# Optimization experiments

Measured on AMD Instinct MI355X. Metric: run time of the kernel, lower is better.

## Reference

```python
import jax, jax.numpy as jnp
import numpy as np

NEG_INF = -1e30
EPS = 1e-7  # keras.backend.epsilon()


def _ctc_loss(y_true, y_pred):
    """Faithful CTC loss matching keras ctc_batch_cost + tf v1 ctc_loss.

    y_true: [B, L] int labels (no blanks), all rows full length L.
    y_pred: [B, T, C] probabilities; tf ctc_loss re-softmaxes log(p+eps).
    Blank index = C - 1. Returns loss [B, 1].
    """
    B, T, C = y_pred.shape
    L = y_true.shape[1]
    S = 2 * L + 1
    blank = C - 1

    # keras passes log(y_pred+eps) as logits; tf ctc_loss applies softmax
    lp = jax.nn.log_softmax(jnp.log(y_pred + EPS), axis=-1)  # [B,T,C]

    # extended label sequence: blank, l0, blank, l1, ..., blank  [B,S]
    ext = jnp.full((B, S), blank, dtype=y_true.dtype)
    ext = ext.at[:, 1::2].set(y_true)

    # skip transition (s-2 -> s) allowed iff ext[s] != blank and ext[s] != ext[s-2]
    same_as_2back = jnp.concatenate(
        [jnp.ones((B, 2), bool), ext[:, 2:] == ext[:, :-2]], axis=1)
    can_skip = (ext != blank) & (~same_as_2back)  # [B,S]

    # emission log-prob of each lattice state at each time: [B,T,S]
    lp_ext = jnp.take_along_axis(lp, ext[:, None, :], axis=2)

    # alpha init at t=0: only states 0 (blank) and 1 (first label) reachable
    alpha0 = jnp.full((B, S), NEG_INF, dtype=lp.dtype)
    alpha0 = alpha0.at[:, 0].set(lp_ext[:, 0, 0])
    alpha0 = alpha0.at[:, 1].set(lp_ext[:, 0, 1])

    pad1 = jnp.full((B, 1), NEG_INF, dtype=lp.dtype)
    pad2 = jnp.full((B, 2), NEG_INF, dtype=lp.dtype)

    def step(alpha, lp_t):
        a_stay = alpha
        a_prev = jnp.concatenate([pad1, alpha[:, :-1]], axis=1)
        a_skip = jnp.where(can_skip,
                           jnp.concatenate([pad2, alpha[:, :-2]], axis=1),
                           NEG_INF)
        m = jnp.maximum(a_stay, jnp.maximum(a_prev, a_skip))
        lse = m + jnp.log(jnp.exp(a_stay - m) + jnp.exp(a_prev - m)
                          + jnp.exp(a_skip - m))
        return lse + lp_t, None

    # scan over remaining T-1 time steps
    alphaT, _ = jax.lax.scan(step, alpha0, jnp.swapaxes(lp_ext, 0, 1)[1:])

    # total log-likelihood: end at last blank or last label
    loglik = jnp.logaddexp(alphaT[:, S - 1], alphaT[:, S - 2])
    return -loglik[:, None]  # [B,1], matches expand_dims(..., 1)


def setup_inputs() -> dict:
    key = jax.random.key(0)
    k1, k2 = jax.random.split(key)
    B, T, C, L = 128, 1024, 128, 128
    y_true = jax.random.randint(k1, (B, L), 0, C - 1, dtype=jnp.int32)
    y_pred = jax.random.uniform(k2, (B, T, C), dtype=jnp.float32)
    return {"y_true": y_true, "y_pred": y_pred}


def reference(y_true, y_pred):
    return _ctc_loss(y_true, y_pred)
```

## Files before the change

kernel.cpp:

```cpp
#include <hip/hip_runtime.h>

#define TT 1024
#define CC 128
#define LL 128
#define EPSF 1e-7f
#define LN2F 0.69314718055994531f

#define LOG2F(x) __builtin_amdgcn_logf(x)

typedef unsigned int uint;

template <int CTRL>
__device__ __forceinline__ int dpp_i(int old_, int x) {
  return __builtin_amdgcn_update_dpp(old_, x, CTRL, 0xf, 0xf, false);
}
__device__ __forceinline__ float dpp_shr1_f32(float x) {
  return __uint_as_float((uint)__builtin_amdgcn_update_dpp(
      0, (int)__float_as_uint(x), 0x138, 0xf, 0xf, true));
}

__device__ __forceinline__ uint bf16bits(float x) {
  uint u = __float_as_uint(x);
  return (u + 0x7fffu + ((u >> 16) & 1u)) >> 16;
}

__device__ __forceinline__ float bperm(int byteaddr, float v) {
  return __uint_as_float(
      (uint)__builtin_amdgcn_ds_bpermute(byteaddr, (int)__float_as_uint(v)));
}


#define CTC_STEP(wv, pbf)                                   \
  do {                                                      \
    const float p1 = __uint_as_float((wv) << 16);           \
    const float p2 = __uint_as_float((wv) & 0xffff0000u);   \
    const float pb = (pbf);                                 \
    const float p3 = dpp_shr1_f32(a3);                      \
    const float n0 = (a0 + p3) * pb;                        \
    const float n1 = __builtin_fmaf(s1f, p3, a0 + a1) * p1; \
    const float n2 = (a2 + a1) * pb;                        \
    const float n3 = __builtin_fmaf(s3f, a1, a3 + a2) * p2; \
    const float n4 = (a4 + a3) * pb;                        \
    a0 = n0; a1 = n1; a2 = n2; a3 = n3; a4 = n4;            \
  } while (0)

#define CTC_QUAD(et, eb)      \
  do {                        \
    CTC_STEP((et).x, (eb).x); \
    CTC_STEP((et).y, (eb).y); \
    CTC_STEP((et).z, (eb).z); \
    CTC_STEP((et).w, (eb).w); \
  } while (0)

#define CTC_RESCALE()                                                \
  do {                                                               \
    const float m = fmaxf(fmaxf(fmaxf(a0, a1), fmaxf(a2, a3)), a4);  \
    int ke = (int)(__float_as_uint(m) >> 23);                        \
    ke = max(ke, dpp_i<0x111>(ke, ke));                              \
    ke = max(ke, dpp_i<0x112>(ke, ke));                              \
    ke = max(ke, dpp_i<0x114>(ke, ke));                              \
    ke = max(ke, dpp_i<0x118>(ke, ke));                              \
    ke = max(ke, dpp_i<0x142>(ke, ke));                              \
    ke = max(ke, dpp_i<0x143>(ke, ke));                              \
    ke = __builtin_amdgcn_readlane(ke, 63);                          \
    int e = ke - 227;             \
    e = e < -127 ? -127 : e;                                         \
    const float sc = __uint_as_float((uint)(127 - e) << 23);         \
    a0 *= sc; a1 *= sc; a2 *= sc; a3 *= sc; a4 *= sc;                \
    ell += e;                                                        \
  } while (0)

#define STAGE8(t0)                                                          \
  do {                                                                      \
    float2 vv[8];                                                           \
    _Pragma("unroll") for (int j = 0; j < 8; ++j)                           \
        vv[j] = *(const float2*)(Pb + (size_t)((t0) + j) * CC);             \
    _Pragma("unroll") for (int q = 0; q < 2; ++q) {                         \
      uint wds[4];                                                          \
      float nys[4];                                                         \
      _Pragma("unroll") for (int c = 0; c < 4; ++c) {                       \
        const int j = q * 4 + c;                                            \
        float x = (vv[j].x + EPSF) + (vv[j].y + EPSF);                      \
        _Pragma("unroll") for (int off = 32; off > 0; off >>= 1)            \
            x += __shfl_xor(x, off);                                        \
        const float r = 1.0f / x;                                           \
        const float er = EPSF * r;                                          \
        const float nx = __builtin_fmaf(vv[j].x, r, er);                    \
        const float ny = __builtin_fmaf(vv[j].y, r, er);                    \
        const float c1a = bperm(gxb, nx), c1b = bperm(gxb, ny);             \
        const float c2a = bperm(gyb, nx), c2b = bperm(gyb, ny);             \
        const float g1 = sx ? c1b : c1a;                                    \
        const float g2 = sy ? c2b : c2a;                                    \
        wds[c] = (bf16bits(g2) << 16) | bf16bits(g1);                       \
        nys[c] = ny;                                                        \
      }                                                                     \
      const int tq = (t0) + q * 4;                                          \
      uint4 val;                                                            \
      val.x = wds[0]; val.y = wds[1]; val.z = wds[2]; val.w = wds[3];       \
      *(uint4*)((char*)ETl + ((tq >> 5) & 3) * 8192 +                       \
                ((tq >> 2) & 7) * 1024 + L * 16) = val;                     \
      if (L == 63) {                                                        \
        float4 e4;                                                          \
        e4.x = nys[0]; e4.y = nys[1]; e4.z = nys[2]; e4.w = nys[3];         \
        *(float4*)&EBl[tq] = e4;                                            \
      }                                                                     \
    }                                                                       \
  } while (0)

__global__ __launch_bounds__(320) void ctc_fused(const int* __restrict__ yt,
                                                 const float* __restrict__ yp,
                                                 float* __restrict__ out) {
  const int b = blockIdx.x;
  const int tid = threadIdx.x;
  const int L = tid & 63;
  const int w = tid >> 6;

  __shared__ uint4 ETl[4][8][64];
  __shared__ __align__(16) float EBl[TT];

  const int2 lab = *(const int2*)(yt + b * LL + 2 * L);

  const int labm1 = __shfl_up(lab.y, 1);
  const float s1f = ((L > 0) && (lab.x != labm1)) ? 1.0f : 0.0f;
  const float s3f = (lab.y != lab.x) ? 1.0f : 0.0f;

  const float* Pb = yp + (size_t)b * TT * CC + 2 * L;
  const int gxb = (lab.x >> 1) << 2, gyb = (lab.y >> 1) << 2;
  const int sx = lab.x & 1, sy = lab.y & 1;

  if (w != 0) {
    STAGE8((w - 1) * 8);
    STAGE8(32 + (w - 1) * 8);
  }
  __syncthreads();

  uint4 etA = {0, 0, 0, 0}, etB = {0, 0, 0, 0};
  float4 ebA = {0, 0, 0, 0}, ebB = {0, 0, 0, 0};
  if (w == 0) {
    etA = ((const uint4*)ETl)[L];
    ebA = *(const float4*)&EBl[0];
  }

  float a0 = (w == 0 && L == 0) ? 0x1.0p100f : 0.0f;
  float a1 = 0.0f, a2 = 0.0f, a3 = 0.0f, a4 = 0.0f;
  int ell = -100;

#pragma unroll 1
  for (int kk = 0; kk < 32; ++kk) {
    if (w == 0) {
      const uint4* cur = (const uint4*)ETl + (size_t)(kk & 3) * 512;
      const float4* ebp = (const float4*)&EBl[kk * 32];
      etB = cur[1 * 64 + L]; ebB = ebp[1];
      CTC_QUAD(etA, ebA);
      etA = cur[2 * 64 + L]; ebA = ebp[2];
      CTC_QUAD(etB, ebB);
      etB = cur[3 * 64 + L]; ebB = ebp[3];
      CTC_QUAD(etA, ebA);
      etA = cur[4 * 64 + L]; ebA = ebp[4];
      CTC_QUAD(etB, ebB);
      CTC_RESCALE();
      etB = cur[5 * 64 + L]; ebB = ebp[5];
      CTC_QUAD(etA, ebA);
      etA = cur[6 * 64 + L]; ebA = ebp[6];
      CTC_QUAD(etB, ebB);
      etB = cur[7 * 64 + L]; ebB = ebp[7];
      CTC_QUAD(etA, ebA);
      etA = ((const uint4*)ETl)[(size_t)((kk + 1) & 3) * 512 + L];
      ebA = *(const float4*)&EBl[(kk < 31) ? (kk + 1) * 32 : 1020];
      CTC_QUAD(etB, ebB);
      CTC_RESCALE();
    } else if (kk < 30) {
      STAGE8((kk + 2) * 32 + (w - 1) * 8);
    }
    __syncthreads();
  }

  if (tid == 63) {
    float s = a3 + a4;
    if (s < 1e-37f) s = 1e-37f;
    out[b] = -LN2F * ((float)ell + LOG2F(s));
  }
}

extern "C" void kernel_launch(void* const* d_in, const int* in_sizes, int n_in,
                              void* d_out, int out_size, void* d_ws,
                              size_t ws_size, hipStream_t stream) {
  (void)d_ws; (void)ws_size; (void)n_in; (void)out_size;
  const int* yt = (const int*)d_in[0];
  const float* yp = (const float*)d_in[1];
  float* out = (float*)d_out;
  const int B = in_sizes[0] / LL;
  hipLaunchKernelGGL(ctc_fused, dim3(B), dim3(320), 0, stream, yt, yp, out);
}
```

Before: 155.6 us.

## Use direct label gathers and DPP row-sum, cut producer waves to three

The staging path stops permuting normalized probabilities across lanes with ds_bpermute. Each lane now loads its two label columns straight from global memory. The row sum over 128 classes uses a DPP reduction plus readlane instead of xor shuffles, with four rows batched for more instruction parallelism. The block shrinks from five waves to four (one recurrence wave, three producers), and work is redistributed in 4-row groups. The aim is lower per-row staging latency, so fewer producer waves can keep up with the alpha recurrence, at the cost of extra scattered global loads and less producer parallelism.

New measurement: 149.7 us. 1.04x faster.

```diff
diff --git a/kernel.cpp b/kernel.cpp
--- a/kernel.cpp
+++ b/kernel.cpp
@@ -14,19 +14,23 @@
 __device__ __forceinline__ int dpp_i(int old_, int x) {
   return __builtin_amdgcn_update_dpp(old_, x, CTRL, 0xf, 0xf, false);
 }
+template <int CTRL>
+__device__ __forceinline__ float dpp0f(float x) {
+  return __uint_as_float((uint)__builtin_amdgcn_update_dpp(
+      0, (int)__float_as_uint(x), CTRL, 0xf, 0xf, true));
+}
 __device__ __forceinline__ float dpp_shr1_f32(float x) {
   return __uint_as_float((uint)__builtin_amdgcn_update_dpp(
       0, (int)__float_as_uint(x), 0x138, 0xf, 0xf, true));
 }
+__device__ __forceinline__ float readlane63_f(float v) {
+  return __uint_as_float(
+      (uint)__builtin_amdgcn_readlane((int)__float_as_uint(v), 63));
+}
 
 __device__ __forceinline__ uint bf16bits(float x) {
   uint u = __float_as_uint(x);
   return (u + 0x7fffu + ((u >> 16) & 1u)) >> 16;
-}
-
-__device__ __forceinline__ float bperm(int byteaddr, float v) {
-  return __uint_as_float(
-      (uint)__builtin_amdgcn_ds_bpermute(byteaddr, (int)__float_as_uint(v)));
 }
 
 
@@ -70,44 +74,55 @@
     ell += e;                                                        \
   } while (0)
 
-#define STAGE8(t0)                                                          \
-  do {                                                                      \
-    float2 vv[8];                                                           \
-    _Pragma("unroll") for (int j = 0; j < 8; ++j)                           \
-        vv[j] = *(const float2*)(Pb + (size_t)((t0) + j) * CC);             \
-    _Pragma("unroll") for (int q = 0; q < 2; ++q) {                         \
-      uint wds[4];                                                          \
-      float nys[4];                                                         \
-      _Pragma("unroll") for (int c = 0; c < 4; ++c) {                       \
-        const int j = q * 4 + c;                                            \
-        float x = (vv[j].x + EPSF) + (vv[j].y + EPSF);                      \
-        _Pragma("unroll") for (int off = 32; off > 0; off >>= 1)            \
-            x += __shfl_xor(x, off);                                        \
-        const float r = 1.0f / x;                                           \
-        const float er = EPSF * r;                                          \
-        const float nx = __builtin_fmaf(vv[j].x, r, er);                    \
-        const float ny = __builtin_fmaf(vv[j].y, r, er);                    \
-        const float c1a = bperm(gxb, nx), c1b = bperm(gxb, ny);             \
-        const float c2a = bperm(gyb, nx), c2b = bperm(gyb, ny);             \
-        const float g1 = sx ? c1b : c1a;                                    \
-        const float g2 = sy ? c2b : c2a;                                    \
-        wds[c] = (bf16bits(g2) << 16) | bf16bits(g1);                       \
-        nys[c] = ny;                                                        \
-      }                                                                     \
-      const int tq = (t0) + q * 4;                                          \
-      uint4 val;                                                            \
-      val.x = wds[0]; val.y = wds[1]; val.z = wds[2]; val.w = wds[3];       \
-      *(uint4*)((char*)ETl + ((tq >> 5) & 3) * 8192 +                       \
-                ((tq >> 2) & 7) * 1024 + L * 16) = val;                     \
-      if (L == 63) {                                                        \
-        float4 e4;                                                          \
-        e4.x = nys[0]; e4.y = nys[1]; e4.z = nys[2]; e4.w = nys[3];         \
-        *(float4*)&EBl[tq] = e4;                                            \
-      }                                                                     \
-    }                                                                       \
-  } while (0)
-
-__global__ __launch_bounds__(320) void ctc_fused(const int* __restrict__ yt,
+#define STAGE4(qg)                                                        \
+  do {                                                                    \
+    const int t0 = (qg) * 4;                                              \
+    float2 vv[4];                                                         \
+    float gx[4], gy[4];                                                   \
+    _Pragma("unroll") for (int j = 0; j < 4; ++j) {                       \
+      const float* Pr = Pb + (size_t)(t0 + j) * CC;                       \
+      vv[j] = *(const float2*)(Pr + 2 * L);                               \
+      gx[j] = Pr[labx];                                                   \
+      gy[j] = Pr[laby];                                                   \
+    }                                                                     \
+    float ss[4];                                                          \
+    _Pragma("unroll") for (int j = 0; j < 4; ++j)                         \
+        ss[j] = (vv[j].x + vv[j].y) + (2.0f * EPSF);                      \
+    _Pragma("unroll") for (int j = 0; j < 4; ++j)                         \
+        ss[j] += dpp0f<0x111>(ss[j]);                      \
+    _Pragma("unroll") for (int j = 0; j < 4; ++j)                         \
+        ss[j] += dpp0f<0x112>(ss[j]);                      \
+    _Pragma("unroll") for (int j = 0; j < 4; ++j)                         \
+        ss[j] += dpp0f<0x114>(ss[j]);                      \
+    _Pragma("unroll") for (int j = 0; j < 4; ++j)                         \
+        ss[j] += dpp0f<0x118>(ss[j]);                      \
+    _Pragma("unroll") for (int j = 0; j < 4; ++j)                         \
+        ss[j] += dpp0f<0x142>(ss[j]);                    \
+    _Pragma("unroll") for (int j = 0; j < 4; ++j)                         \
+        ss[j] += dpp0f<0x143>(ss[j]);  \
+    uint wds[4];                                                          \
+    float nys[4];                                                         \
+    _Pragma("unroll") for (int j = 0; j < 4; ++j) {                       \
+      const float x = readlane63_f(ss[j]);                                \
+      const float r = 1.0f / x;                                           \
+      const float er = EPSF * r;                                          \
+      const float g1 = __builtin_fmaf(gx[j], r, er);                      \
+      const float g2 = __builtin_fmaf(gy[j], r, er);                      \
+      wds[j] = (bf16bits(g2) << 16) | bf16bits(g1);                       \
+      nys[j] = __builtin_fmaf(vv[j].y, r, er);                            \
+    }                                                                     \
+    uint4 val;                                                            \
+    val.x = wds[0]; val.y = wds[1]; val.z = wds[2]; val.w = wds[3];       \
+    *(uint4*)((char*)ETl + (((qg) >> 3) & 3) * 8192 +                     \
+              ((qg) & 7) * 1024 + L * 16) = val;                          \
+    if (L == 63) {                                                        \
+      float4 e4;                                                          \
+      e4.x = nys[0]; e4.y = nys[1]; e4.z = nys[2]; e4.w = nys[3];         \
+      *(float4*)&EBl[t0] = e4;                                            \
+    }                                                                     \
+  } while (0)
+
+__global__ __launch_bounds__(256) void ctc_fused(const int* __restrict__ yt,
                                                  const float* __restrict__ yp,
                                                  float* __restrict__ out) {
   const int b = blockIdx.x;
@@ -124,13 +139,11 @@
   const float s1f = ((L > 0) && (lab.x != labm1)) ? 1.0f : 0.0f;
   const float s3f = (lab.y != lab.x) ? 1.0f : 0.0f;
 
-  const float* Pb = yp + (size_t)b * TT * CC + 2 * L;
-  const int gxb = (lab.x >> 1) << 2, gyb = (lab.y >> 1) << 2;
-  const int sx = lab.x & 1, sy = lab.y & 1;
+  const float* Pb = yp + (size_t)b * TT * CC;
+  const int labx = lab.x, laby = lab.y;
 
   if (w != 0) {
-    STAGE8((w - 1) * 8);
-    STAGE8(32 + (w - 1) * 8);
+    for (int q = w - 1; q < 16; q += 3) STAGE4(q);
   }
   __syncthreads();
 
@@ -170,7 +183,7 @@
       CTC_QUAD(etB, ebB);
       CTC_RESCALE();
     } else if (kk < 30) {
-      STAGE8((kk + 2) * 32 + (w - 1) * 8);
+      for (int q = w - 1; q < 8; q += 3) STAGE4((kk + 2) * 8 + q);
     }
     __syncthreads();
   }
@@ -190,5 +203,5 @@
   const float* yp = (const float*)d_in[1];
   float* out = (float*)d_out;
   const int B = in_sizes[0] / LL;
-  hipLaunchKernelGGL(ctc_fused, dim3(B), dim3(320), 0, stream, yt, yp, out);
-}
+  hipLaunchKernelGGL(ctc_fused, dim3(B), dim3(256), 0, stream, yt, yp, out);
+}
```
